# Kernel tuning notes

Hardware: AMD Instinct MI355X
Metric: run time of the kernel (lower is better)

Reference implementation:

```python
import jax, jax.numpy as jnp
import numpy as np


def setup_inputs() -> dict:
    key = jax.random.key(0)
    k1, k2, k3, k4, k5 = jax.random.split(key, 5)
    B, H, W, C, F = 8, 64, 64, 256, 64
    # glorot_uniform for 1x1 conv kernels [1,1,Cin,Cout]
    def glorot(k, cin, cout):
        lim = float(np.sqrt(6.0 / (cin + cout)))
        return jax.random.uniform(k, (1, 1, cin, cout), jnp.float32, -lim, lim)
    x = jax.random.normal(k1, (B, H, W, C), dtype=jnp.float32)
    Wf = glorot(k2, C, F)
    Wg = glorot(k3, C, F)
    Wh = glorot(k4, C, C)
    Wv = glorot(k5, C, C)
    gamma = jnp.zeros((1,), dtype=jnp.float32) + 0.1  # nonzero so attention path matters
    return {"x": x, "Wf": Wf, "Wg": Wg, "Wh": Wh, "Wv": Wv, "gamma": gamma}


def reference(x, Wf, Wg, Wh, Wv, gamma):
    B, H, W, C = x.shape
    N = H * W
    # 1x1 convs are pointwise matmuls over channels
    f = jnp.einsum('bhwc,cf->bhwf', x, Wf[0, 0])   # [B,H,W,F]
    g = jnp.einsum('bhwc,cf->bhwf', x, Wg[0, 0])   # [B,H,W,F]
    h = jnp.einsum('bhwc,cd->bhwd', x, Wh[0, 0])   # [B,H,W,C]
    ff = f.reshape(B, N, -1)                        # [B,N,F]
    gf = g.reshape(B, N, -1)                        # [B,N,F]
    hf = h.reshape(B, N, C)                         # [B,N,C]
    # s[b,i,j] = ff[b,i,:] . gf[b,j,:]  (no 1/sqrt(d) scaling, as in source)
    s = jnp.einsum('bif,bjf->bij', ff, gf)          # [B,N,N]
    beta = jax.nn.softmax(s, axis=-1)
    o = jnp.einsum('bij,bjc->bic', beta, hf)        # [B,N,C]
    o = o.reshape(B, H, W, C)
    o = jnp.einsum('bhwc,cd->bhwd', o, Wv[0, 0])
    return gamma * o + x
```

## Files before the change

kernel.cpp:

```cpp
#include <hip/hip_runtime.h>

typedef _Float16 half8   __attribute__((ext_vector_type(8)));
typedef _Float16 half4_t __attribute__((ext_vector_type(4)));
typedef float    float4_t __attribute__((ext_vector_type(4)));

#define B_   8
#define N_   4096
#define C_   256
#define F_   64

#if defined(__has_builtin) && __has_builtin(__builtin_amdgcn_exp2f)
#define EXP2(x) __builtin_amdgcn_exp2f(x)
#else
#define EXP2(x) exp2f(x)
#endif
#define LOG2E 1.44269504f

static __device__ __forceinline__ float4_t mfma16(half8 a, half8 b, float4_t c) {
  return __builtin_amdgcn_mfma_f32_16x16x32_f16(a, b, c, 0, 0, 0);
}

template <int CTRL>
static __device__ __forceinline__ float dpp_f(float x) {
  return __int_as_float(__builtin_amdgcn_update_dpp(
      __float_as_int(x), __float_as_int(x), CTRL, 0xF, 0xF, false));
}
static __device__ __forceinline__ float row_max16(float v) {
  v = fmaxf(v, dpp_f<0x128>(v));
  v = fmaxf(v, dpp_f<0x124>(v));
  v = fmaxf(v, dpp_f<0x122>(v));
  v = fmaxf(v, dpp_f<0x121>(v));
  return v;
}
static __device__ __forceinline__ float row_sum16(float v) {
  v += dpp_f<0x128>(v);
  v += dpp_f<0x124>(v);
  v += dpp_f<0x122>(v);
  v += dpp_f<0x121>(v);
  return v;
}

__global__ __launch_bounds__(256) void prep_kernel(const float* __restrict__ Wh,
                                                   const float* __restrict__ Wv,
                                                   const float* __restrict__ Wf,
                                                   const float* __restrict__ Wg,
                                                   _Float16* __restrict__ whvt,
                                                   _Float16* __restrict__ wfgt) {
  int c = threadIdx.x;
  if (blockIdx.x < 256) {
    int d = blockIdx.x;
    const float4_t* whr = (const float4_t*)(Wh + (size_t)c * 256);
    float acc = 0.f;
#pragma unroll 8
    for (int e4 = 0; e4 < 64; ++e4) {
      float4_t w4 = whr[e4];
      acc += w4[0] * Wv[(e4 * 4 + 0) * 256 + d];
      acc += w4[1] * Wv[(e4 * 4 + 1) * 256 + d];
      acc += w4[2] * Wv[(e4 * 4 + 2) * 256 + d];
      acc += w4[3] * Wv[(e4 * 4 + 3) * 256 + d];
    }
    whvt[d * 256 + c] = (_Float16)acc;
  } else {
    int n = blockIdx.x - 256;
    float v = (n < 64) ? Wf[c * 64 + n] * LOG2E : Wg[c * 64 + (n - 64)];
    wfgt[n * 256 + c] = (_Float16)v;
  }
}

__global__ __launch_bounds__(256) void fgt_kernel(const float* __restrict__ x,
                                                  const _Float16* __restrict__ wfgt,
                                                  _Float16* __restrict__ f,
                                                  _Float16* __restrict__ g,
                                                  _Float16* __restrict__ xT) {
  __shared__ float tile[32][33];
  int tid  = threadIdx.x;
  int wave = tid >> 6, lane = tid & 63;
  int n16  = lane & 15, quad = lane >> 4;
  int row  = blockIdx.x * 64 + wave * 16 + n16;
  float4_t acc[8];
#pragma unroll
  for (int t = 0; t < 8; t++) acc[t] = (float4_t){0.f, 0.f, 0.f, 0.f};
  for (int k0 = 0; k0 < 256; k0 += 32) {
    const float* xp = x + (size_t)row * C_ + k0 + quad * 8;
    float4_t x0 = *(const float4_t*)xp;
    float4_t x1 = *(const float4_t*)(xp + 4);
    half8 af;
#pragma unroll
    for (int j = 0; j < 4; j++) { af[j] = (_Float16)x0[j]; af[4 + j] = (_Float16)x1[j]; }
#pragma unroll
    for (int t = 0; t < 8; t++) {
      half8 bf = *(const half8*)(wfgt + (size_t)(t * 16 + n16) * 256 + k0 + quad * 8);
      acc[t] = mfma16(af, bf, acc[t]);
    }
  }
  int orow = blockIdx.x * 64 + wave * 16 + quad * 4;
#pragma unroll
  for (int t = 0; t < 8; t++) {
#pragma unroll
    for (int r = 0; r < 4; r++) {
      _Float16 v = (_Float16)acc[t][r];
      int col = t * 16 + n16;
      if (t < 4) f[(size_t)(orow + r) * 64 + col] = v;
      else       g[(size_t)(orow + r) * 64 + col - 64] = v;
    }
  }

  const int b   = blockIdx.x >> 6;
  const int nb  = (blockIdx.x & 63) << 6;
  const int tr  = tid >> 3;
  const int tc  = (tid & 7) << 2;
#pragma unroll 1
  for (int s = 0; s < 16; ++s) {
    const int n0 = nb + ((s & 1) << 5);
    const int c0 = (s >> 1) << 5;
    __syncthreads();
    const float* src = x + ((size_t)(b * N_ + n0 + tr)) * C_ + c0 + tc;
    float4_t v = *(const float4_t*)src;
    tile[tr][tc + 0] = v[0]; tile[tr][tc + 1] = v[1];
    tile[tr][tc + 2] = v[2]; tile[tr][tc + 3] = v[3];
    __syncthreads();
    half4_t o;
    o[0] = (_Float16)tile[tc + 0][tr];
    o[1] = (_Float16)tile[tc + 1][tr];
    o[2] = (_Float16)tile[tc + 2][tr];
    o[3] = (_Float16)tile[tc + 3][tr];
    _Float16* dst = xT + ((size_t)(b * C_ + c0 + tr)) * N_ + n0 + tc;
    *(half4_t*)dst = o;
  }
}

__global__ __launch_bounds__(256, 2) void flash_kernel(const _Float16* __restrict__ f,
                                                       const _Float16* __restrict__ g,
                                                       const _Float16* __restrict__ xT,
                                                       _Float16* __restrict__ a) {
  __shared__ _Float16 ktb2[2][64 * 64];
  __shared__ _Float16 ptb2[2][64 * 64];
  __shared__ float alpha_lds[2][64];
  __shared__ float linv_lds[64];

  const int b   = blockIdx.x;
  const int i0  = blockIdx.y * 64;
  const int tid = threadIdx.x;
  const int wave = tid >> 6, lane = tid & 63;
  const int n16 = lane & 15, quad = lane >> 4;
  const int nlo = n16 & 7, nhi = n16 >> 3;

  half8 qf[2];
  {
    const _Float16* qp = f + (size_t)(b * N_ + i0 + wave * 16 + n16) * 64 + quad * 8;
    qf[0] = *(const half8*)qp;
    qf[1] = *(const half8*)(qp + 32);
  }

  float4_t o_acc[16];
#pragma unroll
  for (int t = 0; t < 16; t++) o_acc[t] = (float4_t){0.f, 0.f, 0.f, 0.f};
  float m_i[4] = {-1e30f, -1e30f, -1e30f, -1e30f};
  float l_i[4] = {0.f, 0.f, 0.f, 0.f};

  const _Float16* gbase = g + (size_t)(b * N_) * 64;
  const _Float16* xbase = xT + ((size_t)b * C_ + 64 * wave) * (size_t)N_;

  const int krow = tid >> 2;
  const int kcb  = (tid & 3) << 1;
  const int krb  = krow & 7;

  {
    const _Float16* ks = gbase + (size_t)krow * 64 + (kcb << 3);
    half8 k0 = *(const half8*)ks;
    half8 k1 = *(const half8*)(ks + 8);
    _Float16* kd = ktb2[0] + krow * 64;
    *(half8*)(kd + (((kcb    ) ^ krb) << 3)) = k0;
    *(half8*)(kd + (((kcb + 1) ^ krb) << 3)) = k1;
  }
  __syncthreads();

  for (int k = 0; k < 64; ++k) {
    const int j0  = k << 6;
    const int buf = k & 1;
    const int j0n = (j0 + 64) & (N_ - 1);

    half8 kp0, kp1;
    {
      const _Float16* ks = gbase + (size_t)(j0n + krow) * 64 + (kcb << 3);
      kp0 = *(const half8*)ks;
      kp1 = *(const half8*)(ks + 8);
    }
    half8 vfr[8];
#pragma unroll
    for (int s = 0; s < 2; s++)
#pragma unroll
      for (int ct = 0; ct < 4; ct++)
        vfr[s * 4 + ct] = *(const half8*)(xbase + (size_t)(16 * ct + n16) * N_ +
                                          j0 + 32 * s + 8 * quad);

    float4_t s_acc[4];
#pragma unroll
    for (int t = 0; t < 4; t++) s_acc[t] = (float4_t){0.f, 0.f, 0.f, 0.f};
    {
      const _Float16* ktb = ktb2[buf];
      __builtin_amdgcn_s_setprio(1);
#pragma unroll
      for (int s = 0; s < 2; s++)
#pragma unroll
        for (int t = 0; t < 4; t++) {
          half8 bf = *(const half8*)(ktb + (16 * t + n16) * 64 +
                                     (((4 * s + quad) ^ nlo) << 3));
          s_acc[t] = mfma16(qf[s], bf, s_acc[t]);
        }
      __builtin_amdgcn_s_setprio(0);
    }

    float alpha_r[4];
#pragma unroll
    for (int r = 0; r < 4; r++) {
      float v = fmaxf(fmaxf(s_acc[0][r], s_acc[1][r]),
                      fmaxf(s_acc[2][r], s_acc[3][r]));
      v = row_max16(v);
      float mn = fmaxf(m_i[r], v);
      alpha_r[r] = EXP2(m_i[r] - mn);
      m_i[r] = mn;
    }
    _Float16* pb = ptb2[buf];
#pragma unroll
    for (int r = 0; r < 4; r++) {
      float s0 = EXP2(s_acc[0][r] - m_i[r]);
      float s1 = EXP2(s_acc[1][r] - m_i[r]);
      float s2 = EXP2(s_acc[2][r] - m_i[r]);
      float s3 = EXP2(s_acc[3][r] - m_i[r]);
      float v = row_sum16(s0 + s1 + s2 + s3);
      l_i[r] = l_i[r] * alpha_r[r] + v;
      const int row = wave * 16 + 4 * quad + r;
      const int rb  = row & 7;
      _Float16* pr = pb + row * 64 + nlo;
      pr[((nhi    ) ^ rb) << 3] = (_Float16)s0;
      pr[((nhi + 2) ^ rb) << 3] = (_Float16)s1;
      pr[((nhi + 4) ^ rb) << 3] = (_Float16)s2;
      pr[((nhi + 6) ^ rb) << 3] = (_Float16)s3;
    }
    if (n16 == 0) {
#pragma unroll
      for (int r = 0; r < 4; r++)
        alpha_lds[buf][wave * 16 + 4 * quad + r] = alpha_r[r];
    }
    {
      _Float16* kd = ktb2[buf ^ 1] + krow * 64;
      *(half8*)(kd + (((kcb    ) ^ krb) << 3)) = kp0;
      *(half8*)(kd + (((kcb + 1) ^ krb) << 3)) = kp1;
    }
    __syncthreads();

#pragma unroll
    for (int ti = 0; ti < 4; ti++)
#pragma unroll
      for (int r = 0; r < 4; r++) {
        float al = alpha_lds[buf][ti * 16 + 4 * quad + r];
#pragma unroll
        for (int ct = 0; ct < 4; ct++) o_acc[ti * 4 + ct][r] *= al;
      }

    __builtin_amdgcn_s_setprio(1);
#pragma unroll
    for (int s = 0; s < 2; s++)
#pragma unroll
      for (int ti = 0; ti < 4; ti++) {
        half8 af = *(const half8*)(pb + (16 * ti + n16) * 64 +
                                   (((4 * s + quad) ^ nlo) << 3));
#pragma unroll
        for (int ct = 0; ct < 4; ct++)
          o_acc[ti * 4 + ct] = mfma16(af, vfr[s * 4 + ct], o_acc[ti * 4 + ct]);
      }
    __builtin_amdgcn_s_setprio(0);
  }

  if (n16 == 0) {
#pragma unroll
    for (int r = 0; r < 4; r++)
      linv_lds[wave * 16 + 4 * quad + r] = 1.f / l_i[r];
  }
  __syncthreads();
#pragma unroll
  for (int ti = 0; ti < 4; ti++)
#pragma unroll
    for (int r = 0; r < 4; r++) {
      float il = linv_lds[ti * 16 + 4 * quad + r];
      size_t orow = (size_t)(b * N_ + i0 + ti * 16 + 4 * quad + r) * C_;
#pragma unroll
      for (int ct = 0; ct < 4; ct++)
        a[orow + 64 * wave + 16 * ct + n16] =
            (_Float16)(o_acc[ti * 4 + ct][r] * il);
    }
}

__global__ __launch_bounds__(256) void out_kernel(const _Float16* __restrict__ a,
                                                  const _Float16* __restrict__ whvt,
                                                  const float* __restrict__ x,
                                                  const float* __restrict__ gamma,
                                                  float* __restrict__ out) {
  int tid  = threadIdx.x;
  int wave = tid >> 6, lane = tid & 63;
  int n16  = lane & 15, quad = lane >> 4;
  int row  = blockIdx.x * 64 + wave * 16 + n16;
  int col0 = blockIdx.y * 64;
  float4_t acc[4];
#pragma unroll
  for (int t = 0; t < 4; t++) acc[t] = (float4_t){0.f, 0.f, 0.f, 0.f};
  for (int k0 = 0; k0 < 256; k0 += 32) {
    half8 af = *(const half8*)(a + (size_t)row * C_ + k0 + quad * 8);
#pragma unroll
    for (int t = 0; t < 4; t++) {
      half8 bf = *(const half8*)(whvt +
                  (size_t)(col0 + t * 16 + n16) * 256 + k0 + quad * 8);
      acc[t] = mfma16(af, bf, acc[t]);
    }
  }
  float gm = gamma[0];
  int orow = blockIdx.x * 64 + wave * 16 + quad * 4;
#pragma unroll
  for (int t = 0; t < 4; t++) {
#pragma unroll
    for (int r = 0; r < 4; r++) {
      size_t idx = (size_t)(orow + r) * C_ + col0 + t * 16 + n16;
      out[idx] = gm * acc[t][r] + x[idx];
    }
  }
}

extern "C" void kernel_launch(void* const* d_in, const int* in_sizes, int n_in,
                              void* d_out, int out_size, void* d_ws, size_t ws_size,
                              hipStream_t stream) {
  const float* x     = (const float*)d_in[0];
  const float* Wf    = (const float*)d_in[1];
  const float* Wg    = (const float*)d_in[2];
  const float* Wh    = (const float*)d_in[3];
  const float* Wv    = (const float*)d_in[4];
  const float* gamma = (const float*)d_in[5];
  float* out = (float*)d_out;

  char* w = (char*)d_ws;
  _Float16* whvt = (_Float16*)(w);
  _Float16* wfgt = (_Float16*)(w + 131072);
  _Float16* fb   = (_Float16*)(w + 196608);
  _Float16* gb   = (_Float16*)(w + 196608 + 4194304);
  _Float16* xT   = (_Float16*)(w + 196608 + 2 * 4194304);
  _Float16* ab   = (_Float16*)(w + 196608 + 2 * 4194304 + 16777216);

  hipLaunchKernelGGL(prep_kernel, dim3(384),   dim3(256), 0, stream,
                     Wh, Wv, Wf, Wg, whvt, wfgt);
  hipLaunchKernelGGL(fgt_kernel,  dim3(512),   dim3(256), 0, stream,
                     x, wfgt, fb, gb, xT);
  hipLaunchKernelGGL(flash_kernel, dim3(8, 64), dim3(256), 0, stream, fb, gb, xT, ab);
  hipLaunchKernelGGL(out_kernel,  dim3(512, 4), dim3(256), 0, stream,
                     ab, whvt, x, gamma, out);
}
```

Measured before the change: 287.0 us.

## Stage K tiles via direct global-to-LDS loads and widen transpose steps

The flash kernel now prefetches the next K tile with global_load_lds, writing straight from global memory into shared memory with the XOR swizzle applied on the source side. This replaces the register round-trip and the explicit LDS stores. The intent is to free VGPRs and VALU/LDS-store slots in the main loop. Separately, the x transpose in fgt_kernel handles two 32-channel tiles per iteration, halving the barrier count. The risk is that correctness depends on the async LDS writes being complete at the existing __syncthreads, which may need a vmcnt wait.

```diff
diff --git a/kernel.cpp b/kernel.cpp
--- a/kernel.cpp
+++ b/kernel.cpp
@@ -38,6 +38,23 @@
   v += dpp_f<0x122>(v);
   v += dpp_f<0x121>(v);
   return v;
+}
+
+static __device__ __forceinline__ void stage_k(const _Float16* gsrc,
+                                               _Float16* kd,
+                                               int wave, int lane) {
+  const int srow = lane >> 3;
+  const int sblk = (lane & 7) ^ srow;
+  const _Float16* s = gsrc + (size_t)(wave * 16 + srow) * 64 + (sblk << 3);
+  _Float16* d = kd + (wave * 16) * 64;
+  __builtin_amdgcn_global_load_lds(
+      (const __attribute__((address_space(1))) unsigned int*)s,
+      (__attribute__((address_space(3))) unsigned int*)d, 16, 0, 0);
+  s += 8 * 64;
+  d += 8 * 64;
+  __builtin_amdgcn_global_load_lds(
+      (const __attribute__((address_space(1))) unsigned int*)s,
+      (__attribute__((address_space(3))) unsigned int*)d, 16, 0, 0);
 }
 
 __global__ __launch_bounds__(256) void prep_kernel(const float* __restrict__ Wh,
@@ -72,7 +89,7 @@
                                                   _Float16* __restrict__ f,
                                                   _Float16* __restrict__ g,
                                                   _Float16* __restrict__ xT) {
-  __shared__ float tile[32][33];
+  __shared__ float tile[2][32][33];
   int tid  = threadIdx.x;
   int wave = tid >> 6, lane = tid & 63;
   int n16  = lane & 15, quad = lane >> 4;
@@ -110,22 +127,28 @@
   const int tr  = tid >> 3;
   const int tc  = (tid & 7) << 2;
 #pragma unroll 1
-  for (int s = 0; s < 16; ++s) {
-    const int n0 = nb + ((s & 1) << 5);
-    const int c0 = (s >> 1) << 5;
+  for (int s = 0; s < 8; ++s) {
+    const int n0  = nb + ((s & 1) << 5);
+    const int c0p = (s >> 1) << 6;
     __syncthreads();
-    const float* src = x + ((size_t)(b * N_ + n0 + tr)) * C_ + c0 + tc;
-    float4_t v = *(const float4_t*)src;
-    tile[tr][tc + 0] = v[0]; tile[tr][tc + 1] = v[1];
-    tile[tr][tc + 2] = v[2]; tile[tr][tc + 3] = v[3];
+#pragma unroll
+    for (int h = 0; h < 2; ++h) {
+      const float* src = x + ((size_t)(b * N_ + n0 + tr)) * C_ + c0p + h * 32 + tc;
+      float4_t v = *(const float4_t*)src;
+      tile[h][tr][tc + 0] = v[0]; tile[h][tr][tc + 1] = v[1];
+      tile[h][tr][tc + 2] = v[2]; tile[h][tr][tc + 3] = v[3];
+    }
     __syncthreads();
-    half4_t o;
-    o[0] = (_Float16)tile[tc + 0][tr];
-    o[1] = (_Float16)tile[tc + 1][tr];
-    o[2] = (_Float16)tile[tc + 2][tr];
-    o[3] = (_Float16)tile[tc + 3][tr];
-    _Float16* dst = xT + ((size_t)(b * C_ + c0 + tr)) * N_ + n0 + tc;
-    *(half4_t*)dst = o;
+#pragma unroll
+    for (int h = 0; h < 2; ++h) {
+      half4_t o;
+      o[0] = (_Float16)tile[h][tc + 0][tr];
+      o[1] = (_Float16)tile[h][tc + 1][tr];
+      o[2] = (_Float16)tile[h][tc + 2][tr];
+      o[3] = (_Float16)tile[h][tc + 3][tr];
+      _Float16* dst = xT + ((size_t)(b * C_ + c0p + h * 32 + tr)) * N_ + n0 + tc;
+      *(half4_t*)dst = o;
+    }
   }
 }
 
@@ -161,18 +184,7 @@
   const _Float16* gbase = g + (size_t)(b * N_) * 64;
   const _Float16* xbase = xT + ((size_t)b * C_ + 64 * wave) * (size_t)N_;
 
-  const int krow = tid >> 2;
-  const int kcb  = (tid & 3) << 1;
-  const int krb  = krow & 7;
-
-  {
-    const _Float16* ks = gbase + (size_t)krow * 64 + (kcb << 3);
-    half8 k0 = *(const half8*)ks;
-    half8 k1 = *(const half8*)(ks + 8);
-    _Float16* kd = ktb2[0] + krow * 64;
-    *(half8*)(kd + (((kcb    ) ^ krb) << 3)) = k0;
-    *(half8*)(kd + (((kcb + 1) ^ krb) << 3)) = k1;
-  }
+  stage_k(gbase, ktb2[0], wave, lane);
   __syncthreads();
 
   for (int k = 0; k < 64; ++k) {
@@ -180,12 +192,8 @@
     const int buf = k & 1;
     const int j0n = (j0 + 64) & (N_ - 1);
 
-    half8 kp0, kp1;
-    {
-      const _Float16* ks = gbase + (size_t)(j0n + krow) * 64 + (kcb << 3);
-      kp0 = *(const half8*)ks;
-      kp1 = *(const half8*)(ks + 8);
-    }
+    stage_k(gbase + (size_t)j0n * 64, ktb2[buf ^ 1], wave, lane);
+
     half8 vfr[8];
 #pragma unroll
     for (int s = 0; s < 2; s++)
@@ -243,11 +251,6 @@
       for (int r = 0; r < 4; r++)
         alpha_lds[buf][wave * 16 + 4 * quad + r] = alpha_r[r];
     }
-    {
-      _Float16* kd = ktb2[buf ^ 1] + krow * 64;
-      *(half8*)(kd + (((kcb    ) ^ krb) << 3)) = kp0;
-      *(half8*)(kd + (((kcb + 1) ^ krb) << 3)) = kp1;
-    }
     __syncthreads();
 
 #pragma unroll
```

After: 312.8 us. +9.0%, slower.
